# Kernel tuning notes

Measured on AMD Instinct MI355X. Metric: run time of the kernel, lower is better.

## Reference

```python
import jax, jax.numpy as jnp
import numpy as np

N_HEAD = 16
EPS = 1e-6

def setup_inputs() -> dict:
    key = jax.random.key(0)
    ks = jax.random.split(key, 5)
    B, S, D = 2, 2048, 1024
    scale = 0.02
    return {
        "hidden_states": jax.random.normal(ks[0], (B, S, D), dtype=jnp.float32),
        "w_q": jax.random.normal(ks[1], (D, D), dtype=jnp.float32) * scale,
        "w_k": jax.random.normal(ks[2], (D, D), dtype=jnp.float32) * scale,
        "w_v": jax.random.normal(ks[3], (D, D), dtype=jnp.float32) * scale,
        "w_o": jax.random.normal(ks[4], (D, D), dtype=jnp.float32) * scale,
        "qk_norm_factor": jnp.float32(1.0 / np.sqrt(D // N_HEAD)),
    }

def reference(hidden_states, w_q, w_k, w_v, w_o, qk_norm_factor):
    B, S, D = hidden_states.shape
    H = N_HEAD
    hd = D // H
    # projections (torch Linear without bias: x @ W^T)
    q = jnp.einsum('bsd,ed->bse', hidden_states, w_q).reshape(B, S, H, hd).transpose(0, 2, 1, 3)
    k = jnp.einsum('bsd,ed->bse', hidden_states, w_k).reshape(B, S, H, hd).transpose(0, 2, 1, 3)
    v = jnp.einsum('bsd,ed->bse', hidden_states, w_v).reshape(B, S, H, hd).transpose(0, 2, 1, 3)
    # hypersphere (QK) normalization
    q = q / (jnp.linalg.norm(q, axis=-1, keepdims=True) + EPS)
    k = k / (jnp.linalg.norm(k, axis=-1, keepdims=True) + EPS)
    # scores [B,H,S,S], learned scale
    scores = jnp.einsum('bhqd,bhkd->bhqk', q, k) * qk_norm_factor
    causal = jnp.tril(jnp.ones((S, S), dtype=bool))
    scores = jnp.where(causal[None, None], scores, jnp.float32(-jnp.inf))
    probs = jax.nn.softmax(scores, axis=-1)
    attn = jnp.einsum('bhqk,bhkd->bhqd', probs, v)
    attn = attn.transpose(0, 2, 1, 3).reshape(B, S, D)
    out = jnp.einsum('bsd,ed->bse', attn, w_o)
    return out
```

## Files before the change

kernel.cpp:

```cpp
#include <hip/hip_runtime.h>
#include <hip/hip_bf16.h>

typedef __attribute__((ext_vector_type(8))) short short8;
typedef __attribute__((ext_vector_type(4))) float floatx4;

union BF8 { short8 v; __hip_bfloat16 b[8]; };
union BF4U { ushort4 u; __hip_bfloat16 b[4]; };

__device__ __forceinline__ short8 load8(const __hip_bfloat16* p) {
    return *reinterpret_cast<const short8*>(p);
}

__device__ __forceinline__ void storeC(float* p, float v) { *p = v; }
__device__ __forceinline__ void storeC(__hip_bfloat16* p, float v) { *p = __float2bfloat16(v); }

__device__ __forceinline__ unsigned pack_bf16(float a, float b) {
    unsigned ua = __float_as_uint(a) + 0x8000u;
    unsigned ub = __float_as_uint(b) + 0x8000u;
    return __builtin_amdgcn_perm(ub, ua, 0x07060302u);
}

__device__ __forceinline__ float exp2_fast(float x) {
#if __has_builtin(__builtin_amdgcn_exp2f)
    return __builtin_amdgcn_exp2f(x);
#else
    return __expf(x * 0.6931471805599453f);
#endif
}

__device__ __forceinline__ void gload_lds16(const __hip_bfloat16* g, __hip_bfloat16* l) {
    __builtin_amdgcn_global_load_lds(
        (const __attribute__((address_space(1))) void*)g,
        (__attribute__((address_space(3))) void*)l, 16, 0, 0);
}

__global__ __launch_bounds__(256) void cast_all(const float* __restrict__ hs,
                                                const float* __restrict__ wq,
                                                const float* __restrict__ wk,
                                                const float* __restrict__ wv,
                                                const float* __restrict__ wo,
                                                __hip_bfloat16* __restrict__ Xb,
                                                __hip_bfloat16* __restrict__ Wb) {
    int i = blockIdx.x * 256 + threadIdx.x;
    const float* src;
    __hip_bfloat16* dst;
    if (blockIdx.y == 0) {
        src = hs; dst = Xb;
    } else {
        int m = i >> 18;
        src = (m == 0) ? wq : (m == 1) ? wk : (m == 2) ? wv : wo;
        src -= (size_t)m * 1048576;
        dst = Wb;
    }
    float4 v = reinterpret_cast<const float4*>(src)[i];
    BF4U u;
    u.b[0] = __float2bfloat16(v.x);
    u.b[1] = __float2bfloat16(v.y);
    u.b[2] = __float2bfloat16(v.z);
    u.b[3] = __float2bfloat16(v.w);
    reinterpret_cast<ushort4*>(dst)[i] = u.u;
}

template <typename OutT>
__global__ __launch_bounds__(256) void gemm_bt(const __hip_bfloat16* __restrict__ A,
                                               const __hip_bfloat16* __restrict__ B0,
                                               OutT* __restrict__ C0,
                                               int N, int Kd,
                                               size_t zsB, size_t zsC,
                                               int normz, const float* __restrict__ scale_p) {
    __shared__ __hip_bfloat16 lA[128 * 32];
    __shared__ __hip_bfloat16 lB[128 * 32];
    const __hip_bfloat16* B = B0 + zsB * blockIdx.z;
    OutT* C = C0 + zsC * blockIdx.z;
    const int t = threadIdx.x;
    const int m0 = blockIdx.x * 128, n0 = blockIdx.y * 128;
    const int w = t >> 6, l = t & 63;
    const int wr = (w >> 1) * 64, wc = (w & 1) * 64;
    const int lr = l & 15, lq = l >> 4;

    const floatx4 zero4 = {0.f, 0.f, 0.f, 0.f};
    floatx4 acc[4][4];
#pragma unroll
    for (int mt = 0; mt < 4; ++mt)
#pragma unroll
        for (int nt = 0; nt < 4; ++nt) acc[mt][nt] = zero4;

    for (int k0 = 0; k0 < Kd; k0 += 32) {
#pragma unroll
        for (int i = 0; i < 2; ++i) {
            int flat = t + i * 256;
            int row = flat >> 2, ch = flat & 3;
            gload_lds16(A + (size_t)(m0 + row) * Kd + k0 + ch * 8, lA + flat * 8);
            gload_lds16(B + (size_t)(n0 + row) * Kd + k0 + ch * 8, lB + flat * 8);
        }
        __syncthreads();
        short8 af[4], bfr[4];
#pragma unroll
        for (int mt = 0; mt < 4; ++mt)
            af[mt] = load8(lA + (wr + mt * 16 + lr) * 32 + lq * 8);
#pragma unroll
        for (int nt = 0; nt < 4; ++nt)
            bfr[nt] = load8(lB + (wc + nt * 16 + lr) * 32 + lq * 8);
#pragma unroll
        for (int mt = 0; mt < 4; ++mt)
#pragma unroll
            for (int nt = 0; nt < 4; ++nt)
                acc[mt][nt] = __builtin_amdgcn_mfma_f32_16x16x32_bf16(
                    af[mt], bfr[nt], acc[mt][nt], 0, 0, 0);
        __syncthreads();
    }

    if (normz && blockIdx.z < 2) {
        const float fac = (blockIdx.z == 0) ? (*scale_p * 1.44269504f) : 1.0f;
#pragma unroll
        for (int mt = 0; mt < 4; ++mt)
#pragma unroll
            for (int r = 0; r < 4; ++r) {
                float ss = 0.f;
#pragma unroll
                for (int nt = 0; nt < 4; ++nt) {
                    float v = acc[mt][nt][r];
                    ss += v * v;
                }
                ss += __shfl_xor(ss, 1, 64);
                ss += __shfl_xor(ss, 2, 64);
                ss += __shfl_xor(ss, 4, 64);
                ss += __shfl_xor(ss, 8, 64);
                float inv = fac / (sqrtf(ss) + 1e-6f);
#pragma unroll
                for (int nt = 0; nt < 4; ++nt) acc[mt][nt][r] *= inv;
            }
    }

#pragma unroll
    for (int mt = 0; mt < 4; ++mt)
#pragma unroll
        for (int nt = 0; nt < 4; ++nt)
#pragma unroll
            for (int r = 0; r < 4; ++r) {
                int row = m0 + wr + mt * 16 + lq * 4 + r;
                int col = n0 + wc + nt * 16 + lr;
                storeC(C + (size_t)row * N + col, acc[mt][nt][r]);
            }
}

__global__ __launch_bounds__(256) void transpose_v(const __hip_bfloat16* __restrict__ V,
                                                   __hip_bfloat16* __restrict__ Vt) {
    const int S = 2048, D = 1024;
    __shared__ __hip_bfloat16 tile[64][72];
    int t = threadIdx.x;
    int s0 = blockIdx.x * 64;
    int bh = blockIdx.y, b = bh >> 4, h = bh & 15;
    const __hip_bfloat16* src = V + ((size_t)b * S) * D + h * 64;
#pragma unroll
    for (int i = 0; i < 2; ++i) {
        int flat = t + i * 256;
        int sr = flat >> 3, ch = flat & 7;
        *reinterpret_cast<short8*>(&tile[sr][ch * 8]) =
            load8(src + (size_t)(s0 + sr) * D + ch * 8);
    }
    __syncthreads();
    __hip_bfloat16* dst = Vt + (size_t)bh * 64 * S;
#pragma unroll
    for (int i = 0; i < 2; ++i) {
        int flat = t + i * 256;
        int d = flat >> 3, sc = flat & 7;
        BF8 u;
#pragma unroll
        for (int j = 0; j < 8; ++j) u.b[j] = tile[sc * 8 + j][d];
        *reinterpret_cast<short8*>(dst + (size_t)d * S + s0 + sc * 8) = u.v;
    }
}

__global__ __launch_bounds__(256) void flash_attn(const __hip_bfloat16* __restrict__ Q,
                                                  const __hip_bfloat16* __restrict__ K,
                                                  const __hip_bfloat16* __restrict__ Vt,
                                                  __hip_bfloat16* __restrict__ O) {
    const int S = 2048, D = 1024;
    __shared__ __align__(16) char smem[20480];
    const int t = threadIdx.x;
    const int w = t >> 6, l = t & 63;
    const int lr = l & 15, lq = l >> 4;
    const int id = blockIdx.x;
    const int bh = (id & 7) * 4 + ((id >> 3) & 3);
    const int pr = id >> 5;
    const int b = bh >> 4, h = bh & 15;
    const __hip_bfloat16* Qb = Q + ((size_t)b * S) * D + h * 64;
    const __hip_bfloat16* Kb = K + ((size_t)b * S) * D + h * 64;
    const __hip_bfloat16* Vb = Vt + (size_t)bh * 64 * S;
    __hip_bfloat16* lPw = reinterpret_cast<__hip_bfloat16*>(smem) + w * (64 * 40);
    float* buf = reinterpret_cast<float*>(smem);

#pragma unroll 1
    for (int tile = 0; tile < 2; ++tile) {
        const int jq = (tile == 0) ? (31 - pr) : pr;
        const int q0 = jq * 64;

        short8 bq[4][2];
#pragma unroll
        for (int nt = 0; nt < 4; ++nt)
#pragma unroll
            for (int kt = 0; kt < 2; ++kt)
                bq[nt][kt] = load8(Qb + (size_t)(q0 + nt * 16 + lr) * D + kt * 32 + lq * 8);

        const floatx4 zero4 = {0.f, 0.f, 0.f, 0.f};
        floatx4 oacc[4][4];
        float lsum[4] = {0.f, 0.f, 0.f, 0.f};
#pragma unroll
        for (int mt = 0; mt < 4; ++mt)
#pragma unroll
            for (int nt = 0; nt < 4; ++nt) oacc[mt][nt] = zero4;

        const int klast = 2 * jq + 1;
        const int kmask = 2 * jq;

        if (w <= klast) {
            short8 bk[2][2], bv[4];
            {
                const int k0 = w * 32;
#pragma unroll
                for (int mt = 0; mt < 2; ++mt)
#pragma unroll
                    for (int kt = 0; kt < 2; ++kt)
                        bk[mt][kt] = load8(Kb + (size_t)(k0 + mt * 16 + lr) * D + kt * 32 + lq * 8);
#pragma unroll
                for (int nt = 0; nt < 4; ++nt)
                    bv[nt] = load8(Vb + (size_t)(nt * 16 + lr) * S + k0 + lq * 8);
            }
            int ks = w;
#pragma unroll 1
            while (true) {
                const int k0 = ks * 32;
                const bool more = (ks + 4) <= klast;
                const int k0n = (more ? (ks + 4) : ks) * 32;
                short8 nk[2][2], nv[4];
#pragma unroll
                for (int mt = 0; mt < 2; ++mt)
#pragma unroll
                    for (int kt = 0; kt < 2; ++kt)
                        nk[mt][kt] = load8(Kb + (size_t)(k0n + mt * 16 + lr) * D + kt * 32 + lq * 8);
#pragma unroll
                for (int nt = 0; nt < 4; ++nt)
                    nv[nt] = load8(Vb + (size_t)(nt * 16 + lr) * S + k0n + lq * 8);
                floatx4 sacc[2][4];
#pragma unroll
                for (int mt = 0; mt < 2; ++mt)
#pragma unroll
                    for (int nt = 0; nt < 4; ++nt) sacc[mt][nt] = zero4;
#pragma unroll
                for (int mt = 0; mt < 2; ++mt)
#pragma unroll
                    for (int nt = 0; nt < 4; ++nt)
#pragma unroll
                        for (int kt = 0; kt < 2; ++kt)
                            sacc[mt][nt] = __builtin_amdgcn_mfma_f32_16x16x32_bf16(
                                bk[mt][kt], bq[nt][kt], sacc[mt][nt], 0, 0, 0);
                const bool domask = ks >= kmask;
#pragma unroll
                for (int mt = 0; mt < 2; ++mt)
#pragma unroll
                    for (int nt = 0; nt < 4; ++nt) {
                        float p0 = exp2_fast(sacc[mt][nt][0]);
                        float p1 = exp2_fast(sacc[mt][nt][1]);
                        float p2 = exp2_fast(sacc[mt][nt][2]);
                        float p3 = exp2_fast(sacc[mt][nt][3]);
                        if (domask) {
                            const int qg = q0 + nt * 16 + lr;
                            const int kb = k0 + mt * 16 + lq * 4;
                            p0 = (kb + 0 <= qg) ? p0 : 0.f;
                            p1 = (kb + 1 <= qg) ? p1 : 0.f;
                            p2 = (kb + 2 <= qg) ? p2 : 0.f;
                            p3 = (kb + 3 <= qg) ? p3 : 0.f;
                        }
                        lsum[nt] += (p0 + p1) + (p2 + p3);
                        uint2 d;
                        d.x = pack_bf16(p0, p1);
                        d.y = pack_bf16(p2, p3);
                        *reinterpret_cast<uint2*>(lPw + (nt * 16 + lr) * 40 + mt * 16 + lq * 4) = d;
                    }
                asm volatile("s_waitcnt lgkmcnt(0)" ::: "memory");
                short8 ap[4];
#pragma unroll
                for (int mtq = 0; mtq < 4; ++mtq)
                    ap[mtq] = load8(lPw + (mtq * 16 + lr) * 40 + lq * 8);
#pragma unroll
                for (int mtq = 0; mtq < 4; ++mtq)
#pragma unroll
                    for (int ntd = 0; ntd < 4; ++ntd)
                        oacc[mtq][ntd] = __builtin_amdgcn_mfma_f32_16x16x32_bf16(
                            ap[mtq], bv[ntd], oacc[mtq][ntd], 0, 0, 0);
                if (!more) break;
                ks += 4;
#pragma unroll
                for (int mt = 0; mt < 2; ++mt)
#pragma unroll
                    for (int kt = 0; kt < 2; ++kt) bk[mt][kt] = nk[mt][kt];
#pragma unroll
                for (int nt = 0; nt < 4; ++nt) bv[nt] = nv[nt];
            }
        }

#pragma unroll
        for (int nt = 0; nt < 4; ++nt) {
            float s = lsum[nt];
            s += __shfl_xor(s, 16, 64);
            s += __shfl_xor(s, 32, 64);
            lsum[nt] = s;
        }

        const int row = t >> 2, c0 = (t & 3) * 4;
        __hip_bfloat16* Ob = O + ((size_t)b * S) * D + h * 64;
        float inv = 0.f;
#pragma unroll 1
        for (int chunk = 0; chunk < 4; ++chunk) {
#pragma unroll
            for (int mtq = 0; mtq < 4; ++mtq)
#pragma unroll
                for (int r = 0; r < 4; ++r)
                    buf[w * 1280 + (mtq * 16 + lq * 4 + r) * 20 + lr] = oacc[mtq][chunk][r];
            if (chunk == 0 && lq == 0) {
#pragma unroll
                for (int nt = 0; nt < 4; ++nt)
                    buf[w * 1280 + (nt * 16 + lr) * 20 + 16] = lsum[nt];
            }
            __syncthreads();
            if (chunk == 0) {
                float Lt = buf[row * 20 + 16] + buf[1280 + row * 20 + 16] +
                           buf[2560 + row * 20 + 16] + buf[3840 + row * 20 + 16];
                inv = 1.f / Lt;
            }
            float4 a = {0.f, 0.f, 0.f, 0.f};
#pragma unroll
            for (int w2 = 0; w2 < 4; ++w2) {
                float4 v = *reinterpret_cast<const float4*>(buf + w2 * 1280 + row * 20 + c0);
                a.x += v.x; a.y += v.y; a.z += v.z; a.w += v.w;
            }
            uint2 d;
            d.x = pack_bf16(a.x * inv, a.y * inv);
            d.y = pack_bf16(a.z * inv, a.w * inv);
            *reinterpret_cast<uint2*>(Ob + (size_t)(q0 + row) * D + chunk * 16 + c0) = d;
            __syncthreads();
        }
    }
}

extern "C" void kernel_launch(void* const* d_in, const int* in_sizes, int n_in,
                              void* d_out, int out_size, void* d_ws, size_t ws_size,
                              hipStream_t stream) {
    const float* hs  = (const float*)d_in[0];
    const float* wq  = (const float*)d_in[1];
    const float* wk  = (const float*)d_in[2];
    const float* wv  = (const float*)d_in[3];
    const float* wo  = (const float*)d_in[4];
    const float* qkf = (const float*)d_in[5];

    char* ws = (char*)d_ws;
    const size_t MB = 1024 * 1024;
    __hip_bfloat16* Xb  = (__hip_bfloat16*)(ws);
    __hip_bfloat16* Wqb = (__hip_bfloat16*)(ws + 8 * MB);
    __hip_bfloat16* Wob = (__hip_bfloat16*)(ws + 14 * MB);
    __hip_bfloat16* Qb  = (__hip_bfloat16*)(ws + 16 * MB);
    __hip_bfloat16* Kb  = (__hip_bfloat16*)(ws + 24 * MB);
    __hip_bfloat16* Vb  = (__hip_bfloat16*)(ws + 32 * MB);
    __hip_bfloat16* Vt  = (__hip_bfloat16*)(ws + 40 * MB);
    __hip_bfloat16* Ab  = (__hip_bfloat16*)(ws + 48 * MB);

    cast_all<<<dim3(4096, 2), 256, 0, stream>>>(hs, wq, wk, wv, wo, Xb, Wqb);

    gemm_bt<__hip_bfloat16><<<dim3(32, 8, 3), 256, 0, stream>>>(
        Xb, Wqb, Qb, 1024, 1024, (size_t)1048576, (size_t)4194304, 1, qkf);

    transpose_v<<<dim3(32, 32), 256, 0, stream>>>(Vb, Vt);
    flash_attn<<<512, 256, 0, stream>>>(Qb, Kb, Vt, Ab);

    gemm_bt<float><<<dim3(32, 8, 1), 256, 0, stream>>>(
        Ab, Wob, (float*)d_out, 1024, 1024, (size_t)0, (size_t)0, 0, qkf);
}
```

Before: 224.9 us.

## Feed softmax probabilities straight from registers into 16x16x16 MFMA, dropping LDS round-trip

The flash attention inner loop no longer writes the bf16 probability tile to LDS and reads it back transposed. The S accumulator layout is reused directly as the A operand of 16x16x16 bf16 MFMAs, with V loaded as 4-element fragments to match. The K/V register double-buffering prefetch is removed, so loads are issued each iteration without software pipelining. A barrier is moved so the epilogue reuse of shared memory stays safe. The change trades the LDS traffic and wait for twice as many smaller MFMA instructions and exposed global-load latency.

```diff
diff --git a/kernel.cpp b/kernel.cpp
--- a/kernel.cpp
+++ b/kernel.cpp
@@ -2,13 +2,18 @@
 #include <hip/hip_bf16.h>
 
 typedef __attribute__((ext_vector_type(8))) short short8;
+typedef __attribute__((ext_vector_type(4))) short short4v;
 typedef __attribute__((ext_vector_type(4))) float floatx4;
 
 union BF8 { short8 v; __hip_bfloat16 b[8]; };
 union BF4U { ushort4 u; __hip_bfloat16 b[4]; };
+union S4U { uint2 u; short4v v; };
 
 __device__ __forceinline__ short8 load8(const __hip_bfloat16* p) {
     return *reinterpret_cast<const short8*>(p);
+}
+__device__ __forceinline__ short4v load4(const __hip_bfloat16* p) {
+    return *reinterpret_cast<const short4v*>(p);
 }
 
 __device__ __forceinline__ void storeC(float* p, float v) { *p = v; }
@@ -27,6 +32,22 @@
     return __expf(x * 0.6931471805599453f);
 #endif
 }
+
+#if __has_builtin(__builtin_amdgcn_mfma_f32_16x16x16_bf16)
+__device__ __forceinline__ floatx4 mfma16(short4v a, short4v b, floatx4 c) {
+    return __builtin_amdgcn_mfma_f32_16x16x16_bf16(a, b, c, 0, 0, 0);
+}
+#elif __has_builtin(__builtin_amdgcn_mfma_f32_16x16x16bf16_1k)
+__device__ __forceinline__ floatx4 mfma16(short4v a, short4v b, floatx4 c) {
+    return __builtin_amdgcn_mfma_f32_16x16x16bf16_1k(a, b, c, 0, 0, 0);
+}
+#else
+__device__ __forceinline__ floatx4 mfma16(short4v a, short4v b, floatx4 c) {
+    asm volatile("v_mfma_f32_16x16x16_bf16 %0, %1, %2, %0"
+                 : "+v"(c) : "v"(a), "v"(b));
+    return c;
+}
+#endif
 
 __device__ __forceinline__ void gload_lds16(const __hip_bfloat16* g, __hip_bfloat16* l) {
     __builtin_amdgcn_global_load_lds(
@@ -188,7 +209,6 @@
     const __hip_bfloat16* Qb = Q + ((size_t)b * S) * D + h * 64;
     const __hip_bfloat16* Kb = K + ((size_t)b * S) * D + h * 64;
     const __hip_bfloat16* Vb = Vt + (size_t)bh * 64 * S;
-    __hip_bfloat16* lPw = reinterpret_cast<__hip_bfloat16*>(smem) + w * (64 * 40);
     float* buf = reinterpret_cast<float*>(smem);
 
 #pragma unroll 1
@@ -215,33 +235,15 @@
         const int kmask = 2 * jq;
 
         if (w <= klast) {
-            short8 bk[2][2], bv[4];
-            {
-                const int k0 = w * 32;
+#pragma unroll 1
+            for (int ks = w; ks <= klast; ks += 4) {
+                const int k0 = ks * 32;
+                short8 bk[2][2];
 #pragma unroll
                 for (int mt = 0; mt < 2; ++mt)
 #pragma unroll
                     for (int kt = 0; kt < 2; ++kt)
                         bk[mt][kt] = load8(Kb + (size_t)(k0 + mt * 16 + lr) * D + kt * 32 + lq * 8);
-#pragma unroll
-                for (int nt = 0; nt < 4; ++nt)
-                    bv[nt] = load8(Vb + (size_t)(nt * 16 + lr) * S + k0 + lq * 8);
-            }
-            int ks = w;
-#pragma unroll 1
-            while (true) {
-                const int k0 = ks * 32;
-                const bool more = (ks + 4) <= klast;
-                const int k0n = (more ? (ks + 4) : ks) * 32;
-                short8 nk[2][2], nv[4];
-#pragma unroll
-                for (int mt = 0; mt < 2; ++mt)
-#pragma unroll
-                    for (int kt = 0; kt < 2; ++kt)
-                        nk[mt][kt] = load8(Kb + (size_t)(k0n + mt * 16 + lr) * D + kt * 32 + lq * 8);
-#pragma unroll
-                for (int nt = 0; nt < 4; ++nt)
-                    nv[nt] = load8(Vb + (size_t)(nt * 16 + lr) * S + k0n + lq * 8);
                 floatx4 sacc[2][4];
 #pragma unroll
                 for (int mt = 0; mt < 2; ++mt)
@@ -255,7 +257,14 @@
                         for (int kt = 0; kt < 2; ++kt)
                             sacc[mt][nt] = __builtin_amdgcn_mfma_f32_16x16x32_bf16(
                                 bk[mt][kt], bq[nt][kt], sacc[mt][nt], 0, 0, 0);
+                short4v bv[2][4];
+#pragma unroll
+                for (int mt = 0; mt < 2; ++mt)
+#pragma unroll
+                    for (int ntd = 0; ntd < 4; ++ntd)
+                        bv[mt][ntd] = load4(Vb + (size_t)(ntd * 16 + lr) * S + k0 + mt * 16 + lq * 4);
                 const bool domask = ks >= kmask;
+                short4v ap[2][4];
 #pragma unroll
                 for (int mt = 0; mt < 2; ++mt)
 #pragma unroll
@@ -273,30 +282,18 @@
                             p3 = (kb + 3 <= qg) ? p3 : 0.f;
                         }
                         lsum[nt] += (p0 + p1) + (p2 + p3);
-                        uint2 d;
-                        d.x = pack_bf16(p0, p1);
-                        d.y = pack_bf16(p2, p3);
-                        *reinterpret_cast<uint2*>(lPw + (nt * 16 + lr) * 40 + mt * 16 + lq * 4) = d;
+                        S4U u;
+                        u.u.x = pack_bf16(p0, p1);
+                        u.u.y = pack_bf16(p2, p3);
+                        ap[mt][nt] = u.v;
                     }
-                asm volatile("s_waitcnt lgkmcnt(0)" ::: "memory");
-                short8 ap[4];
-#pragma unroll
-                for (int mtq = 0; mtq < 4; ++mtq)
-                    ap[mtq] = load8(lPw + (mtq * 16 + lr) * 40 + lq * 8);
-#pragma unroll
-                for (int mtq = 0; mtq < 4; ++mtq)
-#pragma unroll
-                    for (int ntd = 0; ntd < 4; ++ntd)
-                        oacc[mtq][ntd] = __builtin_amdgcn_mfma_f32_16x16x32_bf16(
-                            ap[mtq], bv[ntd], oacc[mtq][ntd], 0, 0, 0);
-                if (!more) break;
-                ks += 4;
-#pragma unroll
-                for (int mt = 0; mt < 2; ++mt)
-#pragma unroll
-                    for (int kt = 0; kt < 2; ++kt) bk[mt][kt] = nk[mt][kt];
-#pragma unroll
-                for (int nt = 0; nt < 4; ++nt) bv[nt] = nv[nt];
+#pragma unroll
+                for (int mt = 0; mt < 2; ++mt)
+#pragma unroll
+                    for (int ntq = 0; ntq < 4; ++ntq)
+#pragma unroll
+                        for (int ntd = 0; ntd < 4; ++ntd)
+                            oacc[ntq][ntd] = mfma16(ap[mt][ntq], bv[mt][ntd], oacc[ntq][ntd]);
             }
         }
 
@@ -311,6 +308,7 @@
         const int row = t >> 2, c0 = (t & 3) * 4;
         __hip_bfloat16* Ob = O + ((size_t)b * S) * D + h * 64;
         float inv = 0.f;
+        __syncthreads();
 #pragma unroll 1
         for (int chunk = 0; chunk < 4; ++chunk) {
 #pragma unroll
@@ -339,7 +337,7 @@
             d.x = pack_bf16(a.x * inv, a.y * inv);
             d.y = pack_bf16(a.z * inv, a.w * inv);
             *reinterpret_cast<uint2*>(Ob + (size_t)(q0 + row) * D + chunk * 16 + c0) = d;
-            __syncthreads();
+            if (chunk < 3) __syncthreads();
         }
     }
 }
```

After: 227.1 us. About the same (+1.0%).
